# Kernel optimization log

Hardware: AMD Instinct MI355X
Metric: run time of the kernel (lower is better)

The kernel has to match this reference:

```python
import jax, jax.numpy as jnp
import numpy as np

B, N, V, X, H, C = 128, 1023, 32000, 256, 256, 10  # N = 2^10 - 1 perfect binary tree (heap layout)


def setup_inputs() -> dict:
    key = jax.random.key(0)
    ks = jax.random.split(key, 12)
    s = 0.02
    return {
        "wordid": jax.random.randint(ks[0], (B, N), 0, V),
        "h0": jnp.zeros((B, N, H), jnp.float32),
        "c0": jnp.zeros((B, N, H), jnp.float32),
        "emb": jax.random.normal(ks[1], (V, X), jnp.float32) * s,
        "W_iou": jax.random.normal(ks[2], (3 * H, X), jnp.float32) * s,
        "U_iou": jax.random.normal(ks[3], (3 * H, 2 * H), jnp.float32) * s,
        "b_iou": jnp.zeros((1, 3 * H), jnp.float32),
        "Uf_W": jax.random.normal(ks[4], (2 * H, 2 * H), jnp.float32) * s,
        "Uf_b": jnp.zeros((2 * H,), jnp.float32),
        "Wmem": jax.random.normal(ks[5], (H, H), jnp.float32) * s,
        "wh_W": jax.random.normal(ks[6], (H, H), jnp.float32) * s,
        "wh_b": jnp.zeros((H,), jnp.float32),
        "lin_W": jax.random.normal(ks[7], (C, H), jnp.float32) * s,
        "lin_b": jnp.zeros((C,), jnp.float32),
    }


def _apply_node(iou, b_iou, c_in):
    # TreeLSTMCell.apply_node_func: iou -> i,o,u gates; c = sig(i)*tanh(u) + c_in; h = sig(o)*tanh(c)
    i, o, u = jnp.split(iou + b_iou, 3, axis=-1)
    c = jax.nn.sigmoid(i) * jnp.tanh(u) + c_in
    h = jax.nn.sigmoid(o) * jnp.tanh(c)
    return h, c


def reference(wordid, h0, c0, emb, W_iou, U_iou, b_iou, Uf_W, Uf_b, Wmem, wh_W, wh_b, lin_W, lin_b):
    Bn, Nn, Hn = h0.shape
    D = int(np.log2(Nn + 1))  # depth of perfect binary tree
    h, c = h0, c0
    # --- leaves (frontier 0): iou = W_iou(embed), c from initial state ---
    s = 2 ** (D - 1) - 1
    x_leaf = emb[wordid[:, s:]]                                  # [B, Nleaf, X]
    iou = jnp.einsum('bnx,gx->bng', x_leaf, W_iou)               # [B, Nleaf, 3H]
    hl, cl = _apply_node(iou, b_iou, c[:, s:])
    h = h.at[:, s:].set(hl)
    c = c.at[:, s:].set(cl)
    # --- internal levels, bottom-up (reduce_func overwrites iou and c) ---
    for level in range(D - 2, -1, -1):
        ps, pe = 2 ** level - 1, 2 ** (level + 1) - 1
        npar = pe - ps
        cs, ce = pe, pe + 2 * npar  # children of parent p live at 2p+1, 2p+2 (contiguous block)
        h_cat = h[:, cs:ce].reshape(Bn, npar, 2 * Hn)            # [B, npar, 2H]
        f = jax.nn.sigmoid(jnp.einsum('bnk,jk->bnj', h_cat, Uf_W) + Uf_b)
        f = f.reshape(Bn, npar, 2, Hn)
        c_sum = jnp.sum(f * c[:, cs:ce].reshape(Bn, npar, 2, Hn), axis=2)
        iou_p = jnp.einsum('bnk,gk->bng', h_cat, U_iou)          # [B, npar, 3H]
        hp, cp = _apply_node(iou_p, b_iou, c_sum)
        h = h.at[:, ps:pe].set(hp)
        c = c.at[:, ps:pe].set(cp)
    # --- TreeAttention: root (node 0 per tree) attends over all nodes of its tree ---
    dec = h[:, 0]                                                # [B, H]
    proj = jnp.einsum('bnh,gh->bng', h, Wmem)                    # memory_project
    scores = jnp.einsum('bh,bnh->bn', dec, proj)
    attn = jax.nn.softmax(scores, axis=1)                        # MaskedSoftmax, mask=None
    context = jnp.einsum('bn,bnh->bh', attn, h)                  # [B, H]
    hid = jax.nn.relu(context @ wh_W.T + wh_b)
    return hid @ lin_W.T + lin_b                                 # [B, num_classes]
```

## Files before the change

### kernel.cpp

```cpp
#include <hip/hip_runtime.h>
#include <math.h>

#define BB      128
#define NNODES  1023
#define HD      256
#define LEAVES  512
#define IOU3    768
#define CAT2    512
#define LDCOMB  1280

typedef unsigned short ushort_t;
typedef __bf16 bf16x8 __attribute__((ext_vector_type(8)));
typedef float  f32x4  __attribute__((ext_vector_type(4)));

__device__ __forceinline__ float sigf(float x) { return 1.0f / (1.0f + expf(-x)); }

__device__ __forceinline__ void gload16(const void* g, void* l)
{
    __builtin_amdgcn_global_load_lds(
        (const __attribute__((address_space(1))) unsigned int*)g,
        (__attribute__((address_space(3))) unsigned int*)l, 16, 0, 0);
}

__device__ __forceinline__ void split_bf16(float x, ushort_t& h, ushort_t& l)
{
    unsigned u = __float_as_uint(x);
    unsigned r = u + 0x7fff + ((u >> 16) & 1);
    h = (ushort_t)(r >> 16);
    float fh = __uint_as_float((unsigned)h << 16);
    float d = x - fh;
    unsigned u2 = __float_as_uint(d);
    unsigned r2 = u2 + 0x7fff + ((u2 >> 16) & 1);
    l = (ushort_t)(r2 >> 16);
}

__device__ __forceinline__ float rh2(ushort_t h, ushort_t l)
{
    return __uint_as_float((unsigned)h << 16) + __uint_as_float((unsigned)l << 16);
}

__global__ void k_split4(const float* __restrict__ src, ushort_t* __restrict__ hi,
                         ushort_t* __restrict__ lo, int n4)
{
    int i = blockIdx.x * 256 + threadIdx.x;
    if (i >= n4) return;
    float4 v = ((const float4*)src)[i];
    ushort4 hv, lv;
    split_bf16(v.x, hv.x, lv.x);
    split_bf16(v.y, hv.y, lv.y);
    split_bf16(v.z, hv.z, lv.z);
    split_bf16(v.w, hv.w, lv.w);
    ((ushort4*)hi)[i] = hv;
    ((ushort4*)lo)[i] = lv;
}

__global__ void k_build_wcat(const float* __restrict__ Uf, const float* __restrict__ Ui,
                             ushort_t* __restrict__ hi, ushort_t* __restrict__ lo)
{
    int i = blockIdx.x * 256 + threadIdx.x;
    if (i >= 1280 * 128) return;
    int row = i >> 7, c4 = i & 127;
    const float* src = (row < 512) ? (Uf + (size_t)row * 512)
                                   : (Ui + (size_t)(row - 512) * 512);
    float4 v = ((const float4*)src)[c4];
    ushort4 hv, lv;
    split_bf16(v.x, hv.x, lv.x);
    split_bf16(v.y, hv.y, lv.y);
    split_bf16(v.z, hv.z, lv.z);
    split_bf16(v.w, hv.w, lv.w);
    ((ushort4*)hi)[i] = hv;
    ((ushort4*)lo)[i] = lv;
}

#define BM 128
#define BN 128
#define BK 32

__global__ __launch_bounds__(512, 4)
void gemm_mfma(const ushort_t* __restrict__ Ahi, const ushort_t* __restrict__ Alo,
               const int* __restrict__ ids,
               int lognpar, unsigned sB, int sP, int m0, int K,
               const ushort_t* __restrict__ Bhi, const ushort_t* __restrict__ Blo,
               float* __restrict__ C, int ldc)
{
    __shared__ __align__(16) char lds[65536];
    const int tid = threadIdx.x;

    int bx = blockIdx.x, by = blockIdx.y;
    {
        const int gx = gridDim.x, gy = gridDim.y;
        if ((gx & 7) == 0) {
            int f = by * gx + bx;
            int span = gy << 3;
            int s = f / span;
            int wv = f - s * span;
            bx = (s << 3) + (wv & 7);
            by = wv >> 3;
        }
    }

    const int w = tid >> 6, lane = tid & 63;

    unsigned aoff, boff;
    {
        int row = tid >> 2;
        int slotp = (tid & 3) ^ ((row >> 1) & 3);
        int mg = m0 + bx * BM + row;
        unsigned ab;
        if (ids) {
            ab = (unsigned)ids[mg] * (unsigned)K;
        } else {
            int b = mg >> lognpar;
            int q = mg & ((1 << lognpar) - 1);
            ab = (unsigned)b * sB + (unsigned)q * (unsigned)sP;
        }
        aoff = ab + slotp * 8;
        boff = (unsigned)(by * BN + row) * (unsigned)K + slotp * 8;
    }
    const int wdst = w * 1024;

    auto STAGE = [&](int k0, char* buf) {
        gload16(Ahi + aoff + k0, buf +     0 + wdst);
        gload16(Alo + aoff + k0, buf +  8192 + wdst);
        gload16(Bhi + boff + k0, buf + 16384 + wdst);
        gload16(Blo + boff + k0, buf + 24576 + wdst);
    };

    const int wm = w >> 2, wn = w & 3;
    const int rA0 = wm * 64 + (lane & 15);
    const int rB0 = wn * 32 + (lane & 15);
    const int ko = lane >> 4;
    const int rdA = rA0 * 64 + ((ko ^ ((rA0 >> 1) & 3)) << 4);
    const int rdB = rB0 * 64 + ((ko ^ ((rB0 >> 1) & 3)) << 4);

    f32x4 acc[4][2];
#pragma unroll
    for (int mi = 0; mi < 4; ++mi)
#pragma unroll
        for (int ni = 0; ni < 2; ++ni) acc[mi][ni] = (f32x4){0.f, 0.f, 0.f, 0.f};

    const int nt = K / BK;
    STAGE(0, lds);
    int cur = 0;
    for (int t = 0; t < nt; ++t) {
        if (t + 1 < nt) {
            STAGE((t + 1) * BK, lds + (cur ^ 1) * 32768);
            asm volatile("s_waitcnt vmcnt(4)" ::: "memory");
        } else {
            asm volatile("s_waitcnt vmcnt(0)" ::: "memory");
        }
        __builtin_amdgcn_s_barrier();
        __builtin_amdgcn_sched_barrier(0);
        char* base = lds + cur * 32768;
        bf16x8 ah[4], al[4], bh[2], bl[2];
#pragma unroll
        for (int f = 0; f < 4; ++f) {
            ah[f] = *(const bf16x8*)(base +        rdA + f * 1024);
            al[f] = *(const bf16x8*)(base + 8192 + rdA + f * 1024);
        }
#pragma unroll
        for (int f = 0; f < 2; ++f) {
            bh[f] = *(const bf16x8*)(base + 16384 + rdB + f * 1024);
            bl[f] = *(const bf16x8*)(base + 24576 + rdB + f * 1024);
        }
        __builtin_amdgcn_s_setprio(1);
#pragma unroll
        for (int mi = 0; mi < 4; ++mi)
#pragma unroll
            for (int ni = 0; ni < 2; ++ni) {
                acc[mi][ni] = __builtin_amdgcn_mfma_f32_16x16x32_bf16(ah[mi], bh[ni], acc[mi][ni], 0, 0, 0);
                acc[mi][ni] = __builtin_amdgcn_mfma_f32_16x16x32_bf16(ah[mi], bl[ni], acc[mi][ni], 0, 0, 0);
                acc[mi][ni] = __builtin_amdgcn_mfma_f32_16x16x32_bf16(al[mi], bh[ni], acc[mi][ni], 0, 0, 0);
            }
        __builtin_amdgcn_s_setprio(0);
        __builtin_amdgcn_s_barrier();
        cur ^= 1;
    }

    {
        char* patch = lds + w * 2304;
        const int cl = lane & 15, rg = lane >> 4;
        const int gcol0 = by * BN + wn * 32;
#pragma unroll
        for (int mi = 0; mi < 4; ++mi) {
#pragma unroll
            for (int ni = 0; ni < 2; ++ni)
#pragma unroll
                for (int r = 0; r < 4; ++r)
                    *(float*)(patch + (rg * 4 + r) * 144 + (ni * 16 + cl) * 4) = acc[mi][ni][r];
            int grow0 = bx * BM + wm * 64 + mi * 16;
#pragma unroll
            for (int i = 0; i < 2; ++i) {
                int slot = lane + 64 * i;
                int lr = slot >> 3, c4 = slot & 7;
                f32x4 vv = *(const f32x4*)(patch + lr * 144 + c4 * 16);
                *(f32x4*)(C + (size_t)(grow0 + lr) * ldc + gcol0 + c4 * 4) = vv;
            }
        }
    }
}

__global__ void k_leaf_ids(const int* __restrict__ wordid, int* __restrict__ ids)
{
    int idx = blockIdx.x * 256 + threadIdx.x;
    int b = idx >> 9, leaf = idx & 511;
    ids[idx] = wordid[b * NNODES + 511 + leaf];
}

__global__ void k_apply_leaf(const float* __restrict__ buf, const float* __restrict__ b_iou,
                             const float* __restrict__ c0,
                             ushort_t* __restrict__ hhi, ushort_t* __restrict__ hlo,
                             float* __restrict__ c, int m0)
{
    int idx = blockIdx.x * 256 + threadIdx.x;
    int m_l = idx >> 8, hh = idx & 255;
    int mg = m0 + m_l;
    int b = mg >> 9, leaf = mg & 511;
    int node = 511 + leaf;
    const float* br = buf + (size_t)m_l * IOU3;
    float iv = br[hh]        + b_iou[hh];
    float ov = br[256 + hh]  + b_iou[256 + hh];
    float uv = br[512 + hh]  + b_iou[512 + hh];
    size_t nb = ((size_t)b * NNODES + node) * HD + hh;
    float cn = sigf(iv) * tanhf(uv) + c0[nb];
    float hn = sigf(ov) * tanhf(cn);
    c[nb] = cn;
    split_bf16(hn, hhi[nb], hlo[nb]);
}

__global__ void k_apply_level(const float* __restrict__ buf, const float* __restrict__ b_iou,
                              const float* __restrict__ Uf_b,
                              ushort_t* __restrict__ hhi, ushort_t* __restrict__ hlo,
                              float* __restrict__ c,
                              int m0, int lognpar, int ps, int cs)
{
    int idx = blockIdx.x * 256 + threadIdx.x;
    int m_l = idx >> 8, hh = idx & 255;
    int mg = m0 + m_l;
    int b = mg >> lognpar;
    int p = mg & ((1 << lognpar) - 1);
    const float* br = buf + (size_t)m_l * LDCOMB;
    float fl = sigf(br[hh]        + Uf_b[hh]);
    float fr = sigf(br[256 + hh]  + Uf_b[256 + hh]);
    size_t cb = ((size_t)b * NNODES + cs + 2 * p) * HD + hh;
    float csum = fl * c[cb] + fr * c[cb + HD];
    float iv = br[512 + hh]  + b_iou[hh];
    float ov = br[768 + hh]  + b_iou[256 + hh];
    float uv = br[1024 + hh] + b_iou[512 + hh];
    float cn = sigf(iv) * tanhf(uv) + csum;
    float hn = sigf(ov) * tanhf(cn);
    size_t pb = ((size_t)b * NNODES + ps + p) * HD + hh;
    c[pb] = cn;
    split_bf16(hn, hhi[pb], hlo[pb]);
}

__global__ void k_dec_v(const ushort_t* __restrict__ hhi, const ushort_t* __restrict__ hlo,
                        const float* __restrict__ Wmem, float* __restrict__ v)
{
    int b = blockIdx.x, k = threadIdx.x;
    __shared__ float dec[HD];
    size_t base = (size_t)b * NNODES * HD;
    dec[k] = rh2(hhi[base + k], hlo[base + k]);
    __syncthreads();
    float s = 0.f;
    for (int g = 0; g < HD; ++g) s = fmaf(dec[g], Wmem[g * HD + k], s);
    v[b * HD + k] = s;
}

__global__ void k_scores(const ushort_t* __restrict__ hhi, const ushort_t* __restrict__ hlo,
                         const float* __restrict__ v, float* __restrict__ scores)
{
    int b = blockIdx.x;
    int w = threadIdx.x >> 6, lane = threadIdx.x & 63;
    int n = blockIdx.y * 4 + w;
    if (n >= NNODES) return;
    size_t hb = ((size_t)b * NNODES + n) * HD;
    ushort4 ph = *(const ushort4*)(hhi + hb + lane * 4);
    ushort4 pl = *(const ushort4*)(hlo + hb + lane * 4);
    float4 vv = *(const float4*)(v + b * HD + lane * 4);
    float s = rh2(ph.x, pl.x) * vv.x + rh2(ph.y, pl.y) * vv.y +
              rh2(ph.z, pl.z) * vv.z + rh2(ph.w, pl.w) * vv.w;
#pragma unroll
    for (int o = 32; o; o >>= 1) s += __shfl_down(s, o);
    if (lane == 0) scores[(size_t)b * NNODES + n] = s;
}

__global__ void k_softmax(const float* __restrict__ scores, float* __restrict__ attn)
{
    int b = blockIdx.x, t = threadIdx.x;
    __shared__ float red[4];
    float sv[4];
    float m = -INFINITY;
#pragma unroll
    for (int i = 0; i < 4; ++i) {
        int n = t + 256 * i;
        sv[i] = (n < NNODES) ? scores[(size_t)b * NNODES + n] : -INFINITY;
        m = fmaxf(m, sv[i]);
    }
#pragma unroll
    for (int o = 32; o; o >>= 1) m = fmaxf(m, __shfl_xor(m, o));
    int w = t >> 6, lane = t & 63;
    if (lane == 0) red[w] = m;
    __syncthreads();
    m = fmaxf(fmaxf(red[0], red[1]), fmaxf(red[2], red[3]));
    float s = 0.f;
#pragma unroll
    for (int i = 0; i < 4; ++i) {
        int n = t + 256 * i;
        sv[i] = (n < NNODES) ? expf(sv[i] - m) : 0.f;
        s += sv[i];
    }
#pragma unroll
    for (int o = 32; o; o >>= 1) s += __shfl_xor(s, o);
    __syncthreads();
    if (lane == 0) red[w] = s;
    __syncthreads();
    s = red[0] + red[1] + red[2] + red[3];
    float inv = 1.0f / s;
#pragma unroll
    for (int i = 0; i < 4; ++i) {
        int n = t + 256 * i;
        if (n < NNODES) attn[(size_t)b * NNODES + n] = sv[i] * inv;
    }
}

__global__ void k_context(const ushort_t* __restrict__ hhi, const ushort_t* __restrict__ hlo,
                          const float* __restrict__ attn, float* __restrict__ partial)
{
    int b = blockIdx.x, ch = blockIdx.y, k = threadIdx.x;
    int n0 = ch * 128;
    int n1 = n0 + 128; if (n1 > NNODES) n1 = NNODES;
    float s = 0.f;
    for (int n = n0; n < n1; ++n) {
        size_t i = ((size_t)b * NNODES + n) * HD + k;
        s = fmaf(attn[(size_t)b * NNODES + n], rh2(hhi[i], hlo[i]), s);
    }
    partial[((size_t)b * 8 + ch) * HD + k] = s;
}

__global__ void k_final(const float* __restrict__ partial,
                        const float* __restrict__ wh_W, const float* __restrict__ wh_b,
                        const float* __restrict__ lin_W, const float* __restrict__ lin_b,
                        float* __restrict__ out)
{
    int b = blockIdx.x, j = threadIdx.x;
    __shared__ float ctx[HD];
    __shared__ float hid[HD];
    float s = 0.f;
#pragma unroll
    for (int ch = 0; ch < 8; ++ch) s += partial[((size_t)b * 8 + ch) * HD + j];
    ctx[j] = s;
    __syncthreads();
    float a = wh_b[j];
    for (int k = 0; k < HD; ++k) a = fmaf(ctx[k], wh_W[j * HD + k], a);
    hid[j] = fmaxf(a, 0.f);
    __syncthreads();
    if (j < 10) {
        float o = lin_b[j];
        for (int k = 0; k < HD; ++k) o = fmaf(hid[k], lin_W[j * HD + k], o);
        out[b * 10 + j] = o;
    }
}

extern "C" void kernel_launch(void* const* d_in, const int* in_sizes, int n_in,
                              void* d_out, int out_size, void* d_ws, size_t ws_size,
                              hipStream_t stream)
{
    const int*   wordid = (const int*)d_in[0];
    const float* c0     = (const float*)d_in[2];
    const float* emb    = (const float*)d_in[3];
    const float* W_iou  = (const float*)d_in[4];
    const float* U_iou  = (const float*)d_in[5];
    const float* b_iou  = (const float*)d_in[6];
    const float* Uf_W   = (const float*)d_in[7];
    const float* Uf_b   = (const float*)d_in[8];
    const float* Wmem   = (const float*)d_in[9];
    const float* wh_W   = (const float*)d_in[10];
    const float* wh_b   = (const float*)d_in[11];
    const float* lin_W  = (const float*)d_in[12];
    const float* lin_b  = (const float*)d_in[13];
    float* out = (float*)d_out;

    const int V = in_sizes[3] / 256;
    const size_t nh = (size_t)BB * NNODES * HD;

    char* ws = (char*)d_ws;
    size_t off = 0;
    auto alloc = [&](size_t bytes) -> void* {
        void* p = ws + off;
        off += (bytes + 255) & ~(size_t)255;
        return p;
    };
    ushort_t* hhi  = (ushort_t*)alloc(nh * 2);
    ushort_t* hlo  = (ushort_t*)alloc(nh * 2);
    float*    c    = (float*)   alloc(nh * 4);
    ushort_t* ehi  = (ushort_t*)alloc((size_t)V * 256 * 2);
    ushort_t* elo  = (ushort_t*)alloc((size_t)V * 256 * 2);
    ushort_t* wchi = (ushort_t*)alloc((size_t)LDCOMB * 512 * 2);
    ushort_t* wclo = (ushort_t*)alloc((size_t)LDCOMB * 512 * 2);
    ushort_t* wihi = (ushort_t*)alloc((size_t)IOU3 * 256 * 2);
    ushort_t* wilo = (ushort_t*)alloc((size_t)IOU3 * 256 * 2);
    int*   ids     = (int*)  alloc((size_t)BB * LEAVES * 4);
    float* v       = (float*)alloc((size_t)BB * HD * 4);
    float* scores  = (float*)alloc((size_t)BB * NNODES * 4);
    float* attn    = (float*)alloc((size_t)BB * NNODES * 4);
    float* partial = (float*)alloc((size_t)BB * 8 * HD * 4);

    size_t remain = (ws_size > off) ? (ws_size - off) : 0;
    size_t rows = remain / (LDCOMB * 4);
    int CH = (int)((rows > 32768) ? 32768 : rows);
    CH &= ~127;
    if (CH < 128) CH = 128;
    float* buf = (float*)alloc((size_t)CH * LDCOMB * 4);

    k_split4<<<(V * 256 / 4 + 255) / 256, 256, 0, stream>>>(emb, ehi, elo, V * 256 / 4);
    k_build_wcat<<<(1280 * 128 + 255) / 256, 256, 0, stream>>>(Uf_W, U_iou, wchi, wclo);
    k_split4<<<(IOU3 * 256 / 4 + 255) / 256, 256, 0, stream>>>(W_iou, wihi, wilo, IOU3 * 256 / 4);
    k_leaf_ids<<<(BB * LEAVES) / 256, 256, 0, stream>>>(wordid, ids);

    {
        int M = BB * LEAVES;
        for (int m0 = 0; m0 < M; m0 += CH) {
            int Mc = M - m0; if (Mc > CH) Mc = CH;
            dim3 g(Mc / BM, IOU3 / BN);
            gemm_mfma<<<g, 512, 0, stream>>>(ehi, elo, ids, 0, 0u, 0, m0, 256,
                                             wihi, wilo, buf, IOU3);
            k_apply_leaf<<<Mc, 256, 0, stream>>>(buf, b_iou, c0, hhi, hlo, c, m0);
        }
    }

    for (int L = 8; L >= 0; --L) {
        int npar = 1 << L;
        int ps = (1 << L) - 1;
        int cs = (1 << (L + 1)) - 1;
        int M = BB * npar;
        unsigned sB = NNODES * HD;
        int sP = 2 * HD;
        const ushort_t* Abh = hhi + (size_t)cs * HD;
        const ushort_t* Abl = hlo + (size_t)cs * HD;
        for (int m0 = 0; m0 < M; m0 += CH) {
            int Mc = M - m0; if (Mc > CH) Mc = CH;
            dim3 g(Mc / BM, LDCOMB / BN);
            gemm_mfma<<<g, 512, 0, stream>>>(Abh, Abl, (const int*)nullptr, L, sB, sP,
                                             m0, CAT2, wchi, wclo, buf, LDCOMB);
            k_apply_level<<<Mc, 256, 0, stream>>>(buf, b_iou, Uf_b, hhi, hlo, c,
                                                  m0, L, ps, cs);
        }
    }

    k_dec_v<<<BB, HD, 0, stream>>>(hhi, hlo, Wmem, v);
    k_scores<<<dim3(BB, 256), 256, 0, stream>>>(hhi, hlo, v, scores);
    k_softmax<<<BB, 256, 0, stream>>>(scores, attn);
    k_context<<<dim3(BB, 8), HD, 0, stream>>>(hhi, hlo, attn, partial);
    k_final<<<BB, HD, 0, stream>>>(partial, wh_W, wh_b, lin_W, lin_b, out);
}
```

Before: 741.0 us.

## Fuse whole tree-LSTM pipeline into one persistent kernel with grid barriers

Replaces the sequence of separate launches (weight splitting, leaf GEMM/apply, per-level GEMM/apply, attention stages) with a single persistent kernel of fixed block count. Stages are separated by an atomic-counter grid barrier. The goal is to remove the launch overhead and tail gaps, which matter most for the small upper tree levels. The risks are spin-wait cost at every barrier, possible deadlock if not all blocks are co-resident, and less parallelism in some stages (fixed grid, dec_v loops serially over k).

```diff
diff --git a/kernel.cpp b/kernel.cpp
--- a/kernel.cpp
+++ b/kernel.cpp
@@ -8,6 +8,7 @@
 #define IOU3    768
 #define CAT2    512
 #define LDCOMB  1280
+#define NBLK    504
 
 typedef unsigned short ushort_t;
 typedef __bf16 bf16x8 __attribute__((ext_vector_type(8)));
@@ -34,72 +35,61 @@
     l = (ushort_t)(r2 >> 16);
 }
 
-__device__ __forceinline__ float rh2(ushort_t h, ushort_t l)
-{
-    return __uint_as_float((unsigned)h << 16) + __uint_as_float((unsigned)l << 16);
-}
-
-__global__ void k_split4(const float* __restrict__ src, ushort_t* __restrict__ hi,
-                         ushort_t* __restrict__ lo, int n4)
-{
-    int i = blockIdx.x * 256 + threadIdx.x;
-    if (i >= n4) return;
-    float4 v = ((const float4*)src)[i];
-    ushort4 hv, lv;
+__device__ __forceinline__ void split4(float4 v, ushort4& hv, ushort4& lv)
+{
     split_bf16(v.x, hv.x, lv.x);
     split_bf16(v.y, hv.y, lv.y);
     split_bf16(v.z, hv.z, lv.z);
     split_bf16(v.w, hv.w, lv.w);
-    ((ushort4*)hi)[i] = hv;
-    ((ushort4*)lo)[i] = lv;
-}
-
-__global__ void k_build_wcat(const float* __restrict__ Uf, const float* __restrict__ Ui,
-                             ushort_t* __restrict__ hi, ushort_t* __restrict__ lo)
-{
-    int i = blockIdx.x * 256 + threadIdx.x;
-    if (i >= 1280 * 128) return;
-    int row = i >> 7, c4 = i & 127;
-    const float* src = (row < 512) ? (Uf + (size_t)row * 512)
-                                   : (Ui + (size_t)(row - 512) * 512);
-    float4 v = ((const float4*)src)[c4];
-    ushort4 hv, lv;
-    split_bf16(v.x, hv.x, lv.x);
-    split_bf16(v.y, hv.y, lv.y);
-    split_bf16(v.z, hv.z, lv.z);
-    split_bf16(v.w, hv.w, lv.w);
-    ((ushort4*)hi)[i] = hv;
-    ((ushort4*)lo)[i] = lv;
+}
+
+__device__ __forceinline__ float rh2(ushort_t h, ushort_t l)
+{
+    return __uint_as_float((unsigned)h << 16) + __uint_as_float((unsigned)l << 16);
+}
+
+__device__ __forceinline__ void gridbar(unsigned* cnt, unsigned* gen)
+{
+    __syncthreads();
+    if (threadIdx.x == 0) {
+        __threadfence();
+        unsigned g = atomicAdd(gen, 0u);
+        if (atomicAdd(cnt, 1u) == (unsigned)gridDim.x - 1u) {
+            atomicExch(cnt, 0u);
+            __threadfence();
+            atomicAdd(gen, 1u);
+        } else {
+            while (atomicAdd(gen, 0u) == g) __builtin_amdgcn_s_sleep(2);
+        }
+        __threadfence();
+    }
+    __syncthreads();
 }
 
 #define BM 128
 #define BN 128
 #define BK 32
 
-__global__ __launch_bounds__(512, 4)
-void gemm_mfma(const ushort_t* __restrict__ Ahi, const ushort_t* __restrict__ Alo,
-               const int* __restrict__ ids,
-               int lognpar, unsigned sB, int sP, int m0, int K,
-               const ushort_t* __restrict__ Bhi, const ushort_t* __restrict__ Blo,
-               float* __restrict__ C, int ldc)
-{
-    __shared__ __align__(16) char lds[65536];
+__device__ __forceinline__ void gemm_tile(char* lds, int f, int gx, int gy,
+    const ushort_t* __restrict__ Ahi, const ushort_t* __restrict__ Alo,
+    const int* __restrict__ wid,
+    int lognpar, unsigned sB, int sP, int m0, int K,
+    const ushort_t* __restrict__ Bhi, const ushort_t* __restrict__ Blo,
+    float* __restrict__ C, int ldc)
+{
+    int bx, by;
+    if ((gx & 7) == 0) {
+        int span = gy << 3;
+        int s = f / span;
+        int wv = f - s * span;
+        bx = (s << 3) + (wv & 7);
+        by = wv >> 3;
+    } else { bx = f % gx; by = f / gx; }
+
     const int tid = threadIdx.x;
-
-    int bx = blockIdx.x, by = blockIdx.y;
-    {
-        const int gx = gridDim.x, gy = gridDim.y;
-        if ((gx & 7) == 0) {
-            int f = by * gx + bx;
-            int span = gy << 3;
-            int s = f / span;
-            int wv = f - s * span;
-            bx = (s << 3) + (wv & 7);
-            by = wv >> 3;
-        }
-    }
-
     const int w = tid >> 6, lane = tid & 63;
+
+    __syncthreads();
 
     unsigned aoff, boff;
     {
@@ -107,8 +97,9 @@
         int slotp = (tid & 3) ^ ((row >> 1) & 3);
         int mg = m0 + bx * BM + row;
         unsigned ab;
-        if (ids) {
-            ab = (unsigned)ids[mg] * (unsigned)K;
+        if (wid) {
+            int b = mg >> 9, lf = mg & 511;
+            ab = (unsigned)wid[b * NNODES + 511 + lf] * (unsigned)K;
         } else {
             int b = mg >> lognpar;
             int q = mg & ((1 << lognpar) - 1);
@@ -154,14 +145,14 @@
         char* base = lds + cur * 32768;
         bf16x8 ah[4], al[4], bh[2], bl[2];
 #pragma unroll
-        for (int f = 0; f < 4; ++f) {
-            ah[f] = *(const bf16x8*)(base +        rdA + f * 1024);
-            al[f] = *(const bf16x8*)(base + 8192 + rdA + f * 1024);
-        }
-#pragma unroll
-        for (int f = 0; f < 2; ++f) {
-            bh[f] = *(const bf16x8*)(base + 16384 + rdB + f * 1024);
-            bl[f] = *(const bf16x8*)(base + 24576 + rdB + f * 1024);
+        for (int q = 0; q < 4; ++q) {
+            ah[q] = *(const bf16x8*)(base +        rdA + q * 1024);
+            al[q] = *(const bf16x8*)(base + 8192 + rdA + q * 1024);
+        }
+#pragma unroll
+        for (int q = 0; q < 2; ++q) {
+            bh[q] = *(const bf16x8*)(base + 16384 + rdB + q * 1024);
+            bl[q] = *(const bf16x8*)(base + 24576 + rdB + q * 1024);
         }
         __builtin_amdgcn_s_setprio(1);
 #pragma unroll
@@ -200,165 +191,223 @@
     }
 }
 
-__global__ void k_leaf_ids(const int* __restrict__ wordid, int* __restrict__ ids)
-{
-    int idx = blockIdx.x * 256 + threadIdx.x;
-    int b = idx >> 9, leaf = idx & 511;
-    ids[idx] = wordid[b * NNODES + 511 + leaf];
-}
-
-__global__ void k_apply_leaf(const float* __restrict__ buf, const float* __restrict__ b_iou,
-                             const float* __restrict__ c0,
-                             ushort_t* __restrict__ hhi, ushort_t* __restrict__ hlo,
-                             float* __restrict__ c, int m0)
-{
-    int idx = blockIdx.x * 256 + threadIdx.x;
-    int m_l = idx >> 8, hh = idx & 255;
-    int mg = m0 + m_l;
-    int b = mg >> 9, leaf = mg & 511;
-    int node = 511 + leaf;
-    const float* br = buf + (size_t)m_l * IOU3;
-    float iv = br[hh]        + b_iou[hh];
-    float ov = br[256 + hh]  + b_iou[256 + hh];
-    float uv = br[512 + hh]  + b_iou[512 + hh];
-    size_t nb = ((size_t)b * NNODES + node) * HD + hh;
-    float cn = sigf(iv) * tanhf(uv) + c0[nb];
-    float hn = sigf(ov) * tanhf(cn);
-    c[nb] = cn;
-    split_bf16(hn, hhi[nb], hlo[nb]);
-}
-
-__global__ void k_apply_level(const float* __restrict__ buf, const float* __restrict__ b_iou,
-                              const float* __restrict__ Uf_b,
-                              ushort_t* __restrict__ hhi, ushort_t* __restrict__ hlo,
-                              float* __restrict__ c,
-                              int m0, int lognpar, int ps, int cs)
-{
-    int idx = blockIdx.x * 256 + threadIdx.x;
-    int m_l = idx >> 8, hh = idx & 255;
-    int mg = m0 + m_l;
-    int b = mg >> lognpar;
-    int p = mg & ((1 << lognpar) - 1);
-    const float* br = buf + (size_t)m_l * LDCOMB;
-    float fl = sigf(br[hh]        + Uf_b[hh]);
-    float fr = sigf(br[256 + hh]  + Uf_b[256 + hh]);
-    size_t cb = ((size_t)b * NNODES + cs + 2 * p) * HD + hh;
-    float csum = fl * c[cb] + fr * c[cb + HD];
-    float iv = br[512 + hh]  + b_iou[hh];
-    float ov = br[768 + hh]  + b_iou[256 + hh];
-    float uv = br[1024 + hh] + b_iou[512 + hh];
-    float cn = sigf(iv) * tanhf(uv) + csum;
-    float hn = sigf(ov) * tanhf(cn);
-    size_t pb = ((size_t)b * NNODES + ps + p) * HD + hh;
-    c[pb] = cn;
-    split_bf16(hn, hhi[pb], hlo[pb]);
-}
-
-__global__ void k_dec_v(const ushort_t* __restrict__ hhi, const ushort_t* __restrict__ hlo,
-                        const float* __restrict__ Wmem, float* __restrict__ v)
-{
-    int b = blockIdx.x, k = threadIdx.x;
-    __shared__ float dec[HD];
-    size_t base = (size_t)b * NNODES * HD;
-    dec[k] = rh2(hhi[base + k], hlo[base + k]);
-    __syncthreads();
-    float s = 0.f;
-    for (int g = 0; g < HD; ++g) s = fmaf(dec[g], Wmem[g * HD + k], s);
-    v[b * HD + k] = s;
-}
-
-__global__ void k_scores(const ushort_t* __restrict__ hhi, const ushort_t* __restrict__ hlo,
-                         const float* __restrict__ v, float* __restrict__ scores)
-{
-    int b = blockIdx.x;
-    int w = threadIdx.x >> 6, lane = threadIdx.x & 63;
-    int n = blockIdx.y * 4 + w;
-    if (n >= NNODES) return;
-    size_t hb = ((size_t)b * NNODES + n) * HD;
-    ushort4 ph = *(const ushort4*)(hhi + hb + lane * 4);
-    ushort4 pl = *(const ushort4*)(hlo + hb + lane * 4);
-    float4 vv = *(const float4*)(v + b * HD + lane * 4);
-    float s = rh2(ph.x, pl.x) * vv.x + rh2(ph.y, pl.y) * vv.y +
-              rh2(ph.z, pl.z) * vv.z + rh2(ph.w, pl.w) * vv.w;
-#pragma unroll
-    for (int o = 32; o; o >>= 1) s += __shfl_down(s, o);
-    if (lane == 0) scores[(size_t)b * NNODES + n] = s;
-}
-
-__global__ void k_softmax(const float* __restrict__ scores, float* __restrict__ attn)
-{
-    int b = blockIdx.x, t = threadIdx.x;
-    __shared__ float red[4];
-    float sv[4];
-    float m = -INFINITY;
-#pragma unroll
-    for (int i = 0; i < 4; ++i) {
-        int n = t + 256 * i;
-        sv[i] = (n < NNODES) ? scores[(size_t)b * NNODES + n] : -INFINITY;
-        m = fmaxf(m, sv[i]);
-    }
-#pragma unroll
-    for (int o = 32; o; o >>= 1) m = fmaxf(m, __shfl_xor(m, o));
-    int w = t >> 6, lane = t & 63;
-    if (lane == 0) red[w] = m;
-    __syncthreads();
-    m = fmaxf(fmaxf(red[0], red[1]), fmaxf(red[2], red[3]));
-    float s = 0.f;
-#pragma unroll
-    for (int i = 0; i < 4; ++i) {
-        int n = t + 256 * i;
-        sv[i] = (n < NNODES) ? expf(sv[i] - m) : 0.f;
-        s += sv[i];
-    }
-#pragma unroll
-    for (int o = 32; o; o >>= 1) s += __shfl_xor(s, o);
-    __syncthreads();
-    if (lane == 0) red[w] = s;
-    __syncthreads();
-    s = red[0] + red[1] + red[2] + red[3];
-    float inv = 1.0f / s;
-#pragma unroll
-    for (int i = 0; i < 4; ++i) {
-        int n = t + 256 * i;
-        if (n < NNODES) attn[(size_t)b * NNODES + n] = sv[i] * inv;
-    }
-}
-
-__global__ void k_context(const ushort_t* __restrict__ hhi, const ushort_t* __restrict__ hlo,
-                          const float* __restrict__ attn, float* __restrict__ partial)
-{
-    int b = blockIdx.x, ch = blockIdx.y, k = threadIdx.x;
-    int n0 = ch * 128;
-    int n1 = n0 + 128; if (n1 > NNODES) n1 = NNODES;
-    float s = 0.f;
-    for (int n = n0; n < n1; ++n) {
-        size_t i = ((size_t)b * NNODES + n) * HD + k;
-        s = fmaf(attn[(size_t)b * NNODES + n], rh2(hhi[i], hlo[i]), s);
-    }
-    partial[((size_t)b * 8 + ch) * HD + k] = s;
-}
-
-__global__ void k_final(const float* __restrict__ partial,
-                        const float* __restrict__ wh_W, const float* __restrict__ wh_b,
-                        const float* __restrict__ lin_W, const float* __restrict__ lin_b,
-                        float* __restrict__ out)
-{
-    int b = blockIdx.x, j = threadIdx.x;
-    __shared__ float ctx[HD];
-    __shared__ float hid[HD];
-    float s = 0.f;
-#pragma unroll
-    for (int ch = 0; ch < 8; ++ch) s += partial[((size_t)b * 8 + ch) * HD + j];
-    ctx[j] = s;
-    __syncthreads();
-    float a = wh_b[j];
-    for (int k = 0; k < HD; ++k) a = fmaf(ctx[k], wh_W[j * HD + k], a);
-    hid[j] = fmaxf(a, 0.f);
-    __syncthreads();
-    if (j < 10) {
-        float o = lin_b[j];
-        for (int k = 0; k < HD; ++k) o = fmaf(hid[k], lin_W[j * HD + k], o);
-        out[b * 10 + j] = o;
+__global__ __launch_bounds__(512, 4)
+void k_tree(const float* __restrict__ emb, const float* __restrict__ W_iou,
+            const float* __restrict__ Uf_W, const float* __restrict__ U_iou,
+            const int* __restrict__ wordid,
+            const float* __restrict__ b_iou, const float* __restrict__ Uf_b,
+            const float* __restrict__ c0, const float* __restrict__ Wmem,
+            const float* __restrict__ wh_W, const float* __restrict__ wh_b,
+            const float* __restrict__ lin_W, const float* __restrict__ lin_b,
+            ushort_t* ehi, ushort_t* elo, ushort_t* wihi, ushort_t* wilo,
+            ushort_t* wchi, ushort_t* wclo,
+            ushort_t* hhi, ushort_t* hlo, float* c,
+            float* buf, float* v, float* scores, float* attn, float* partial,
+            float* out, unsigned* bar, int V)
+{
+    __shared__ __align__(16) char lds[65536];
+    const int tid = threadIdx.x;
+    const unsigned nb = gridDim.x;
+    unsigned* cnt = bar;
+    unsigned* gen = bar + 1;
+
+    {
+        long n4 = (long)V * 64;
+        for (long i = blockIdx.x * 512L + tid; i < n4; i += (long)nb * 512) {
+            ushort4 hv, lv;
+            split4(((const float4*)emb)[i], hv, lv);
+            ((ushort4*)ehi)[i] = hv;
+            ((ushort4*)elo)[i] = lv;
+        }
+        for (int i = blockIdx.x * 512 + tid; i < IOU3 * 64; i += nb * 512) {
+            ushort4 hv, lv;
+            split4(((const float4*)W_iou)[i], hv, lv);
+            ((ushort4*)wihi)[i] = hv;
+            ((ushort4*)wilo)[i] = lv;
+        }
+        for (int i = blockIdx.x * 512 + tid; i < 1280 * 128; i += nb * 512) {
+            int row = i >> 7, c4 = i & 127;
+            const float* src = (row < 512) ? (Uf_W + (size_t)row * 512)
+                                           : (U_iou + (size_t)(row - 512) * 512);
+            ushort4 hv, lv;
+            split4(((const float4*)src)[c4], hv, lv);
+            ((ushort4*)wchi)[i] = hv;
+            ((ushort4*)wclo)[i] = lv;
+        }
+    }
+    gridbar(cnt, gen);
+
+    for (int chk = 0; chk < 2; ++chk) {
+        int m0 = chk * 32768;
+        for (int f = blockIdx.x; f < 256 * 6; f += nb)
+            gemm_tile(lds, f, 256, 6, ehi, elo, wordid, 0, 0u, 0, m0, 256,
+                      wihi, wilo, buf, IOU3);
+        gridbar(cnt, gen);
+        for (long idx = blockIdx.x * 512L + tid; idx < 32768L * 256; idx += (long)nb * 512) {
+            int m_l = (int)(idx >> 8), hh = (int)(idx & 255);
+            int mg = m0 + m_l;
+            int b = mg >> 9, lf = mg & 511;
+            const float* br = buf + (size_t)m_l * IOU3;
+            float iv = br[hh]       + b_iou[hh];
+            float ov = br[256 + hh] + b_iou[256 + hh];
+            float uv = br[512 + hh] + b_iou[512 + hh];
+            size_t nbf = ((size_t)b * NNODES + 511 + lf) * HD + hh;
+            float cn = sigf(iv) * tanhf(uv) + c0[nbf];
+            float hn = sigf(ov) * tanhf(cn);
+            c[nbf] = cn;
+            split_bf16(hn, hhi[nbf], hlo[nbf]);
+        }
+        gridbar(cnt, gen);
+    }
+
+    for (int L = 8; L >= 0; --L) {
+        int npar = 1 << L;
+        int ps = npar - 1, cs = 2 * npar - 1;
+        int gx = npar;
+        int tiles = gx * 10;
+        const ushort_t* Abh = hhi + (size_t)cs * HD;
+        const ushort_t* Abl = hlo + (size_t)cs * HD;
+        for (int f = blockIdx.x; f < tiles; f += nb)
+            gemm_tile(lds, f, gx, 10, Abh, Abl, (const int*)nullptr, L,
+                      (unsigned)(NNODES * HD), 2 * HD, 0, CAT2,
+                      wchi, wclo, buf, LDCOMB);
+        gridbar(cnt, gen);
+        long tot = (long)(BB * npar) * 256;
+        for (long idx = blockIdx.x * 512L + tid; idx < tot; idx += (long)nb * 512) {
+            int m_l = (int)(idx >> 8), hh = (int)(idx & 255);
+            int b = m_l >> L, p = m_l & (npar - 1);
+            const float* br = buf + (size_t)m_l * LDCOMB;
+            float fl = sigf(br[hh]       + Uf_b[hh]);
+            float fr = sigf(br[256 + hh] + Uf_b[256 + hh]);
+            size_t cb = ((size_t)b * NNODES + cs + 2 * p) * HD + hh;
+            float csum = fl * c[cb] + fr * c[cb + HD];
+            float iv = br[512 + hh]  + b_iou[hh];
+            float ov = br[768 + hh]  + b_iou[256 + hh];
+            float uv = br[1024 + hh] + b_iou[512 + hh];
+            float cn = sigf(iv) * tanhf(uv) + csum;
+            float hn = sigf(ov) * tanhf(cn);
+            size_t pb = ((size_t)b * NNODES + ps + p) * HD + hh;
+            c[pb] = cn;
+            split_bf16(hn, hhi[pb], hlo[pb]);
+        }
+        gridbar(cnt, gen);
+    }
+
+    for (int u = blockIdx.x * 512 + tid; u < BB * HD; u += nb * 512) {
+        int b = u >> 8, k = u & 255;
+        size_t base = (size_t)b * NNODES * HD;
+        float s = 0.f;
+        for (int g = 0; g < HD; ++g)
+            s = fmaf(rh2(hhi[base + g], hlo[base + g]), Wmem[g * HD + k], s);
+        v[u] = s;
+    }
+    gridbar(cnt, gen);
+
+    {
+        const int w8 = tid >> 6, lane = tid & 63;
+        for (int u = blockIdx.x; u < BB * 128; u += nb) {
+            int b = u >> 7, ng = u & 127;
+            int n = ng * 8 + w8;
+            if (n < NNODES) {
+                size_t hb = ((size_t)b * NNODES + n) * HD;
+                ushort4 ph = *(const ushort4*)(hhi + hb + lane * 4);
+                ushort4 pl = *(const ushort4*)(hlo + hb + lane * 4);
+                float4 vv = *(const float4*)(v + b * HD + lane * 4);
+                float s = rh2(ph.x, pl.x) * vv.x + rh2(ph.y, pl.y) * vv.y +
+                          rh2(ph.z, pl.z) * vv.z + rh2(ph.w, pl.w) * vv.w;
+#pragma unroll
+                for (int o = 32; o; o >>= 1) s += __shfl_down(s, o);
+                if (lane == 0) scores[(size_t)b * NNODES + n] = s;
+            }
+        }
+    }
+    gridbar(cnt, gen);
+
+    {
+        float* red = (float*)lds;
+        const int w8 = tid >> 6, lane = tid & 63;
+        for (int b = blockIdx.x; b < BB; b += nb) {
+            float sv[2];
+            float m = -INFINITY;
+#pragma unroll
+            for (int i = 0; i < 2; ++i) {
+                int n = tid + 512 * i;
+                sv[i] = (n < NNODES) ? scores[(size_t)b * NNODES + n] : -INFINITY;
+                m = fmaxf(m, sv[i]);
+            }
+#pragma unroll
+            for (int o = 32; o; o >>= 1) m = fmaxf(m, __shfl_xor(m, o));
+            if (lane == 0) red[w8] = m;
+            __syncthreads();
+            m = red[0];
+#pragma unroll
+            for (int i = 1; i < 8; ++i) m = fmaxf(m, red[i]);
+            __syncthreads();
+            float s = 0.f;
+#pragma unroll
+            for (int i = 0; i < 2; ++i) {
+                int n = tid + 512 * i;
+                sv[i] = (n < NNODES) ? expf(sv[i] - m) : 0.f;
+                s += sv[i];
+            }
+#pragma unroll
+            for (int o = 32; o; o >>= 1) s += __shfl_xor(s, o);
+            if (lane == 0) red[w8] = s;
+            __syncthreads();
+            float tot = 0.f;
+#pragma unroll
+            for (int i = 0; i < 8; ++i) tot += red[i];
+            float inv = 1.0f / tot;
+#pragma unroll
+            for (int i = 0; i < 2; ++i) {
+                int n = tid + 512 * i;
+                if (n < NNODES) attn[(size_t)b * NNODES + n] = sv[i] * inv;
+            }
+            __syncthreads();
+        }
+    }
+    gridbar(cnt, gen);
+
+    for (int u = blockIdx.x; u < BB * 16; u += nb) {
+        int b = u >> 4, c2 = u & 15;
+        if (tid < 256) {
+            int n0 = c2 * 64;
+            int n1 = n0 + 64; if (n1 > NNODES) n1 = NNODES;
+            float s = 0.f;
+            for (int n = n0; n < n1; ++n) {
+                size_t i = ((size_t)b * NNODES + n) * HD + tid;
+                s = fmaf(attn[(size_t)b * NNODES + n], rh2(hhi[i], hlo[i]), s);
+            }
+            partial[((size_t)b * 16 + c2) * HD + tid] = s;
+        }
+    }
+    gridbar(cnt, gen);
+
+    {
+        float* ctx = (float*)lds;
+        float* hid = ctx + 256;
+        for (int b = blockIdx.x; b < BB; b += nb) {
+            if (tid < 256) {
+                float s = 0.f;
+#pragma unroll
+                for (int ch = 0; ch < 16; ++ch)
+                    s += partial[((size_t)b * 16 + ch) * HD + tid];
+                ctx[tid] = s;
+            }
+            __syncthreads();
+            if (tid < 256) {
+                float a = wh_b[tid];
+                for (int k = 0; k < HD; ++k) a = fmaf(ctx[k], wh_W[tid * HD + k], a);
+                hid[tid] = fmaxf(a, 0.f);
+            }
+            __syncthreads();
+            if (tid < 10) {
+                float o = lin_b[tid];
+                for (int k = 0; k < HD; ++k) o = fmaf(hid[k], lin_W[tid * HD + k], o);
+                out[b * 10 + tid] = o;
+            }
+            __syncthreads();
+        }
     }
 }
 
@@ -391,6 +440,7 @@
         off += (bytes + 255) & ~(size_t)255;
         return p;
     };
+    unsigned* bar  = (unsigned*)alloc(256);
     ushort_t* hhi  = (ushort_t*)alloc(nh * 2);
     ushort_t* hlo  = (ushort_t*)alloc(nh * 2);
     float*    c    = (float*)   alloc(nh * 4);
@@ -400,57 +450,17 @@
     ushort_t* wclo = (ushort_t*)alloc((size_t)LDCOMB * 512 * 2);
     ushort_t* wihi = (ushort_t*)alloc((size_t)IOU3 * 256 * 2);
     ushort_t* wilo = (ushort_t*)alloc((size_t)IOU3 * 256 * 2);
-    int*   ids     = (int*)  alloc((size_t)BB * LEAVES * 4);
     float* v       = (float*)alloc((size_t)BB * HD * 4);
     float* scores  = (float*)alloc((size_t)BB * NNODES * 4);
     float* attn    = (float*)alloc((size_t)BB * NNODES * 4);
-    float* partial = (float*)alloc((size_t)BB * 8 * HD * 4);
-
-    size_t remain = (ws_size > off) ? (ws_size - off) : 0;
-    size_t rows = remain / (LDCOMB * 4);
-    int CH = (int)((rows > 32768) ? 32768 : rows);
-    CH &= ~127;
-    if (CH < 128) CH = 128;
-    float* buf = (float*)alloc((size_t)CH * LDCOMB * 4);
-
-    k_split4<<<(V * 256 / 4 + 255) / 256, 256, 0, stream>>>(emb, ehi, elo, V * 256 / 4);
-    k_build_wcat<<<(1280 * 128 + 255) / 256, 256, 0, stream>>>(Uf_W, U_iou, wchi, wclo);
-    k_split4<<<(IOU3 * 256 / 4 + 255) / 256, 256, 0, stream>>>(W_iou, wihi, wilo, IOU3 * 256 / 4);
-    k_leaf_ids<<<(BB * LEAVES) / 256, 256, 0, stream>>>(wordid, ids);
-
-    {
-        int M = BB * LEAVES;
-        for (int m0 = 0; m0 < M; m0 += CH) {
-            int Mc = M - m0; if (Mc > CH) Mc = CH;
-            dim3 g(Mc / BM, IOU3 / BN);
-            gemm_mfma<<<g, 512, 0, stream>>>(ehi, elo, ids, 0, 0u, 0, m0, 256,
-                                             wihi, wilo, buf, IOU3);
-            k_apply_leaf<<<Mc, 256, 0, stream>>>(buf, b_iou, c0, hhi, hlo, c, m0);
-        }
-    }
-
-    for (int L = 8; L >= 0; --L) {
-        int npar = 1 << L;
-        int ps = (1 << L) - 1;
-        int cs = (1 << (L + 1)) - 1;
-        int M = BB * npar;
-        unsigned sB = NNODES * HD;
-        int sP = 2 * HD;
-        const ushort_t* Abh = hhi + (size_t)cs * HD;
-        const ushort_t* Abl = hlo + (size_t)cs * HD;
-        for (int m0 = 0; m0 < M; m0 += CH) {
-            int Mc = M - m0; if (Mc > CH) Mc = CH;
-            dim3 g(Mc / BM, LDCOMB / BN);
-            gemm_mfma<<<g, 512, 0, stream>>>(Abh, Abl, (const int*)nullptr, L, sB, sP,
-                                             m0, CAT2, wchi, wclo, buf, LDCOMB);
-            k_apply_level<<<Mc, 256, 0, stream>>>(buf, b_iou, Uf_b, hhi, hlo, c,
-                                                  m0, L, ps, cs);
-        }
-    }
-
-    k_dec_v<<<BB, HD, 0, stream>>>(hhi, hlo, Wmem, v);
-    k_scores<<<dim3(BB, 256), 256, 0, stream>>>(hhi, hlo, v, scores);
-    k_softmax<<<BB, 256, 0, stream>>>(scores, attn);
-    k_context<<<dim3(BB, 8), HD, 0, stream>>>(hhi, hlo, attn, partial);
-    k_final<<<BB, HD, 0, stream>>>(partial, wh_W, wh_b, lin_W, lin_b, out);
-}
+    float* partial = (float*)alloc((size_t)BB * 16 * HD * 4);
+    float* buf     = (float*)alloc((size_t)32768 * LDCOMB * 4);
+    (void)ws_size;
+
+    hipMemsetAsync(bar, 0, 256, stream);
+    k_tree<<<NBLK, 512, 0, stream>>>(
+        emb, W_iou, Uf_W, U_iou, wordid, b_iou, Uf_b, c0, Wmem,
+        wh_W, wh_b, lin_W, lin_b,
+        ehi, elo, wihi, wilo, wchi, wclo,
+        hhi, hlo, c, buf, v, scores, attn, partial, out, bar, V);
+}
```

Result: slower. 2.236 ms (+201.7%).
